# Kernel optimization log

Measured on AMD Instinct MI355X. Metric: run time of the kernel, lower is better.

Reference implementation:

```python
import jax, jax.numpy as jnp
import numpy as np

EPS = 1e-12  # torch F.normalize eps
K = 32       # num_clusters (hardcoded in module)

def l2norm(v, axis):
    n = jnp.sqrt(jnp.sum(v * v, axis=axis, keepdims=True))
    return v / jnp.maximum(n, EPS)

def setup_inputs() -> dict:
    key = jax.random.key(0)
    k1, k2, k3, k4 = jax.random.split(key, 4)
    B, M, D = 64, 128, 2048
    x = jax.random.normal(k1, (B, M, D), dtype=jnp.float32)
    # ragged lengths in [1, M]
    lengths = jax.random.randint(k2, (B,), 0, M, dtype=jnp.int32) + 1
    init_sc = 1.0 / np.sqrt(D)
    W = init_sc * jax.random.normal(k3, (K, D), dtype=jnp.float32)  # fc1.weight
    C = init_sc * jax.random.normal(k4, (K, D), dtype=jnp.float32)  # centroids
    return {"x": x, "lengths": lengths, "W": W, "C": C}

def reference(x, lengths, W, C):
    # x: [B,M,D] padded frames, lengths: [B] valid frame counts
    B, M, D = x.shape
    mask = (jnp.arange(M)[None, :] < lengths[:, None]).astype(x.dtype)  # [B,M]
    cnt = lengths.astype(x.dtype)[:, None]                              # [B,1]
    # avg pooling over valid (raw, un-normalized) frames
    avgpool = jnp.sum(x * mask[:, :, None], axis=1) / cnt               # [B,D]
    # per-frame L2 normalize
    xn = l2norm(x, axis=-1)                                             # [B,M,D]
    # soft assignment: linear (no bias) + softmax over clusters
    logits = jnp.einsum('bmd,kd->bmk', xn, W)
    a = jax.nn.softmax(logits, axis=-1) * mask[:, :, None]              # [B,M,K]
    # VLAD residual aggregation, GEMM form:
    # sum_m a[b,m,k]*(xn[b,m,:] - C[k,:]) = (a^T xn) - C * sum_m a
    ax = jnp.einsum('bmk,bmd->bkd', a, xn)                              # [B,K,D]
    asum = jnp.sum(a, axis=1)                                           # [B,K]
    vlad = ax - asum[:, :, None] * C[None, :, :]                        # [B,K,D]
    # intra-normalize per cluster, flatten, global L2 normalize
    vlad = l2norm(vlad, axis=2)
    vlad = vlad.reshape(B, K * D)
    vlad = l2norm(vlad, axis=1)
    return jnp.concatenate([avgpool, vlad], axis=1)                     # [B, D + K*D]
```

## Files before the change

### kernel.cpp

```cpp
#include <hip/hip_runtime.h>
#include <math.h>

#define BB 64
#define MM 128
#define DDIM 2048
#define KK 32
#define NFR (BB*MM)
#define OUTROW (DDIM + KK*DDIM)

typedef __attribute__((ext_vector_type(8))) short bf16x8;
typedef __attribute__((ext_vector_type(4))) float f32x4;

__device__ __forceinline__ short f2bf(float f) {
  unsigned u = __builtin_bit_cast(unsigned, f);
  u += 0x7fffu + ((u >> 16) & 1u);
  return (short)(u >> 16);
}
__device__ __forceinline__ unsigned pack2(float lo, float hi) {
  return (unsigned)(unsigned short)f2bf(lo) | ((unsigned)(unsigned short)f2bf(hi) << 16);
}

__global__ __launch_bounds__(256) void k_prep(const float* __restrict__ W,
                                              short* __restrict__ Wb) {
  int i = (blockIdx.x * 256 + threadIdx.x) * 8;
  float4 a = *(const float4*)(W + i);
  float4 b = *(const float4*)(W + i + 4);
  bf16x8 o = {f2bf(a.x), f2bf(a.y), f2bf(a.z), f2bf(a.w),
              f2bf(b.x), f2bf(b.y), f2bf(b.z), f2bf(b.w)};
  *(bf16x8*)(Wb + i) = o;
}

__global__ __launch_bounds__(256) void k_logits(const float* __restrict__ x,
    const int* __restrict__ lengths, const short* __restrict__ Wb,
    short* __restrict__ aT, float* __restrict__ asum_p) {
  const int t = threadIdx.x, wv = t >> 6, lane = t & 63;
  const int l15 = lane & 15, quad = lane >> 4;
  const int fg = blockIdx.x;
  const int g0 = fg * 16;
  const int b  = fg >> 3;
  const int m0 = (fg & 7) * 16;
  const int len = lengths[b];

  const float* xrow = x + (size_t)(g0 + l15) * DDIM + wv * 512 + quad * 8;
  const short* w0   = Wb + l15 * DDIM + wv * 512 + quad * 8;
  const short* w1   = w0 + 16 * DDIM;

  f32x4 c0 = {0.f, 0.f, 0.f, 0.f}, c1 = {0.f, 0.f, 0.f, 0.f};
  float ssq = 0.f;
  #pragma unroll
  for (int s = 0; s < 16; ++s) {
    float4 xa = *(const float4*)(xrow + s * 32);
    float4 xc = *(const float4*)(xrow + s * 32 + 4);
    ssq = fmaf(xa.x, xa.x, ssq); ssq = fmaf(xa.y, xa.y, ssq);
    ssq = fmaf(xa.z, xa.z, ssq); ssq = fmaf(xa.w, xa.w, ssq);
    ssq = fmaf(xc.x, xc.x, ssq); ssq = fmaf(xc.y, xc.y, ssq);
    ssq = fmaf(xc.z, xc.z, ssq); ssq = fmaf(xc.w, xc.w, ssq);
    bf16x8 A = {f2bf(xa.x), f2bf(xa.y), f2bf(xa.z), f2bf(xa.w),
                f2bf(xc.x), f2bf(xc.y), f2bf(xc.z), f2bf(xc.w)};
    bf16x8 B0 = *(const bf16x8*)(w0 + s * 32);
    bf16x8 B1 = *(const bf16x8*)(w1 + s * 32);
    c0 = __builtin_amdgcn_mfma_f32_16x16x32_bf16(A, B0, c0, 0, 0, 0);
    c1 = __builtin_amdgcn_mfma_f32_16x16x32_bf16(A, B1, c1, 0, 0, 0);
  }

  ssq += __shfl_xor(ssq, 16, 64);
  ssq += __shfl_xor(ssq, 32, 64);
  __shared__ float sq[4][16];
  __shared__ float lg[4][16][33];
  if (quad == 0) sq[wv][l15] = ssq;
  #pragma unroll
  for (int r = 0; r < 4; ++r) {
    lg[wv][quad * 4 + r][l15]      = c0[r];
    lg[wv][quad * 4 + r][16 + l15] = c1[r];
  }
  __syncthreads();

  const int fr = t >> 4, kk = (t & 15) * 2;
  float s0 = 0.f, s1 = 0.f;
  #pragma unroll
  for (int w = 0; w < 4; ++w) { s0 += lg[w][fr][kk]; s1 += lg[w][fr][kk + 1]; }
  float ss  = sq[0][fr] + sq[1][fr] + sq[2][fr] + sq[3][fr];
  float inv = 1.f / fmaxf(sqrtf(ss), 1e-12f);
  s0 *= inv; s1 *= inv;
  float mx = fmaxf(s0, s1);
  mx = fmaxf(mx, __shfl_xor(mx, 1, 64));
  mx = fmaxf(mx, __shfl_xor(mx, 2, 64));
  mx = fmaxf(mx, __shfl_xor(mx, 4, 64));
  mx = fmaxf(mx, __shfl_xor(mx, 8, 64));
  float e0 = __expf(s0 - mx), e1 = __expf(s1 - mx);
  float se = e0 + e1;
  se += __shfl_xor(se, 1, 64);
  se += __shfl_xor(se, 2, 64);
  se += __shfl_xor(se, 4, 64);
  se += __shfl_xor(se, 8, 64);
  const bool valid = (m0 + fr) < len;
  float rr = valid ? (1.f / se) : 0.f;
  float a0 = e0 * rr, a1 = e1 * rr;

  __syncthreads();
  lg[0][fr][kk] = a0; lg[0][fr][kk + 1] = a1;
  __syncthreads();
  if (t < KK) {
    float s = 0.f;
    #pragma unroll
    for (int f = 0; f < 16; ++f) s += lg[0][f][t];
    asum_p[(size_t)fg * KK + t] = s;
  }
  short* ap = aT + (size_t)b * KK * MM + m0 + fr;
  ap[(size_t)kk * MM]       = f2bf(a0 * inv);
  ap[(size_t)(kk + 1) * MM] = f2bf(a1 * inv);
}

__global__ __launch_bounds__(256) void k_vlad(const float* __restrict__ x,
    const int* __restrict__ lengths, const float* __restrict__ Cc,
    const short* __restrict__ aT, const float* __restrict__ asum_p,
    float* __restrict__ out, float* __restrict__ ssq_part) {
  const int t = threadIdx.x, wv = t >> 6, lane = t & 63;
  const int l15 = lane & 15, quad = lane >> 4;
  const int dc = blockIdx.x, b = blockIdx.y;
  const int dw0 = dc * 256 + wv * 64;
  const int len = lengths[b];

  __shared__ short xbt[4][64][40];
  __shared__ float asl[KK];
  __shared__ float ssw[4][33];

  if (t < KK) {
    float s = 0.f;
    #pragma unroll
    for (int p = 0; p < 8; ++p) s += asum_p[(size_t)(b * 8 + p) * KK + t];
    asl[t] = s;
  }

  const float* xb  = x  + (size_t)b * MM * DDIM;
  const short* at0 = aT + (size_t)b * KK * MM + l15 * MM + quad * 8;

  f32x4 acc[2][4];
  #pragma unroll
  for (int kt = 0; kt < 2; ++kt)
    #pragma unroll
    for (int nt = 0; nt < 4; ++nt) acc[kt][nt] = (f32x4){0.f, 0.f, 0.f, 0.f};
  float avg[4] = {0.f, 0.f, 0.f, 0.f};

  const int q4   = l15 * 4;
  const int mrow = (lane >> 4) * 2;

  for (int ms = 0; ms < 4; ++ms) {
    const int m0 = ms * 32;
    #pragma unroll
    for (int p = 0; p < 4; ++p) {
      int ml = p * 8 + mrow;
      int m  = m0 + ml;
      const float* xr = xb + (size_t)m * DDIM + dw0 + q4;
      float4 v0 = *(const float4*)xr;
      float4 v1 = *(const float4*)(xr + DDIM);
      float f0 = (m < len) ? 1.f : 0.f;
      float f1 = (m + 1 < len) ? 1.f : 0.f;
      avg[0] = fmaf(v0.x, f0, fmaf(v1.x, f1, avg[0]));
      avg[1] = fmaf(v0.y, f0, fmaf(v1.y, f1, avg[1]));
      avg[2] = fmaf(v0.z, f0, fmaf(v1.z, f1, avg[2]));
      avg[3] = fmaf(v0.w, f0, fmaf(v1.w, f1, avg[3]));
      *(unsigned*)&xbt[wv][q4 + 0][ml] = pack2(v0.x, v1.x);
      *(unsigned*)&xbt[wv][q4 + 1][ml] = pack2(v0.y, v1.y);
      *(unsigned*)&xbt[wv][q4 + 2][ml] = pack2(v0.z, v1.z);
      *(unsigned*)&xbt[wv][q4 + 3][ml] = pack2(v0.w, v1.w);
    }
    bf16x8 A0 = *(const bf16x8*)(at0 + m0);
    bf16x8 A1 = *(const bf16x8*)(at0 + 16 * MM + m0);
    #pragma unroll
    for (int nt = 0; nt < 4; ++nt) {
      bf16x8 B = *(const bf16x8*)&xbt[wv][nt * 16 + l15][quad * 8];
      acc[0][nt] = __builtin_amdgcn_mfma_f32_16x16x32_bf16(A0, B, acc[0][nt], 0, 0, 0);
      acc[1][nt] = __builtin_amdgcn_mfma_f32_16x16x32_bf16(A1, B, acc[1][nt], 0, 0, 0);
    }
  }

  #pragma unroll
  for (int c = 0; c < 4; ++c) {
    avg[c] += __shfl_xor(avg[c], 16, 64);
    avg[c] += __shfl_xor(avg[c], 32, 64);
  }
  if (quad == 0) {
    float rl = 1.f / (float)len;
    *(float4*)(out + (size_t)b * OUTROW + dw0 + q4) =
        make_float4(avg[0] * rl, avg[1] * rl, avg[2] * rl, avg[3] * rl);
  }

  __syncthreads();
  float* orow = out + (size_t)b * OUTROW + DDIM;
  #pragma unroll
  for (int kt = 0; kt < 2; ++kt) {
    #pragma unroll
    for (int r = 0; r < 4; ++r) {
      const int k = kt * 16 + quad * 4 + r;
      const float as = asl[k];
      float sqv = 0.f;
      #pragma unroll
      for (int nt = 0; nt < 4; ++nt) {
        const int d = dw0 + nt * 16 + l15;
        float v = acc[kt][nt][r] - as * Cc[(size_t)k * DDIM + d];
        orow[(size_t)k * DDIM + d] = v;
        sqv = fmaf(v, v, sqv);
      }
      sqv += __shfl_xor(sqv, 1, 64);
      sqv += __shfl_xor(sqv, 2, 64);
      sqv += __shfl_xor(sqv, 4, 64);
      sqv += __shfl_xor(sqv, 8, 64);
      if (l15 == 0) ssw[wv][k] = sqv;
    }
  }
  __syncthreads();
  if (t < KK)
    ssq_part[((size_t)dc * BB + b) * KK + t] =
        ssw[0][t] + ssw[1][t] + ssw[2][t] + ssw[3][t];
}

__global__ __launch_bounds__(256) void k_norm(const float* __restrict__ ssq_part,
    float* __restrict__ out) {
  const int t = threadIdx.x;
  const int k = blockIdx.x;
  const int b = blockIdx.y;
  __shared__ float ssk[32];
  if (t < 32) {
    float sk = 0.f;
    #pragma unroll
    for (int dc = 0; dc < 8; ++dc)
      sk += ssq_part[((size_t)dc * BB + b) * KK + t];
    ssk[t] = sk;
  }
  __syncthreads();
  float gss = 0.f, iv_own = 0.f;
  #pragma unroll
  for (int kk = 0; kk < 32; ++kk) {
    float nk = sqrtf(ssk[kk]);
    float iv = 1.f / fmaxf(nk, 1e-12f);
    float nn = nk * iv;
    gss += nn * nn;
    if (kk == k) iv_own = iv;
  }
  float sc = iv_own / fmaxf(sqrtf(gss), 1e-12f);
  float* row = out + (size_t)b * OUTROW + DDIM + (size_t)k * DDIM;
  #pragma unroll
  for (int h = 0; h < 2; ++h) {
    float4* p = (float4*)(row + h * 1024 + t * 4);
    float4 v = *p;
    v.x *= sc; v.y *= sc; v.z *= sc; v.w *= sc;
    *p = v;
  }
}

extern "C" void kernel_launch(void* const* d_in, const int* in_sizes, int n_in,
                              void* d_out, int out_size, void* d_ws, size_t ws_size,
                              hipStream_t stream) {
  const float* x       = (const float*)d_in[0];
  const int*   lengths = (const int*)d_in[1];
  const float* W       = (const float*)d_in[2];
  const float* C       = (const float*)d_in[3];
  float* out = (float*)d_out;

  short* Wb     = (short*)d_ws;
  short* aT     = Wb + (size_t)KK * DDIM;
  float* asum_p = (float*)(aT + (size_t)BB * KK * MM);
  float* ssqp   = asum_p + (size_t)512 * KK;

  k_prep  <<<dim3(32),     256, 0, stream>>>(W, Wb);
  k_logits<<<dim3(512),    256, 0, stream>>>(x, lengths, Wb, aT, asum_p);
  k_vlad  <<<dim3(8, BB),  256, 0, stream>>>(x, lengths, C, aT, asum_p, out, ssqp);
  k_norm  <<<dim3(KK, BB), 256, 0, stream>>>(ssqp, out);
}
```

Before: 146.1 us.

## Fuse W conversion into logits, split VLAD over cluster halves, skip padded frames

Drops the separate W-to-bf16 prep kernel and converts W inline in the logits kernel, which now runs 512 threads per block with each wave covering a narrower D slice. Loads of x for padded frames past each sequence length are skipped in both the logits and VLAD kernels. The VLAD kernel gains a third grid dimension that splits the 32 clusters into two halves, doubling block count but reading x twice. It also adds an XOR swizzle on the shared-memory transpose to reduce bank conflicts and preloads the assignment fragments.

Measured after the change: 176.9 us. +21.1%, slower.

```diff
diff --git a/kernel.cpp b/kernel.cpp
--- a/kernel.cpp
+++ b/kernel.cpp
@@ -16,22 +16,16 @@
   u += 0x7fffu + ((u >> 16) & 1u);
   return (short)(u >> 16);
 }
+__device__ __forceinline__ bf16x8 cvt8(float4 a, float4 b) {
+  return (bf16x8){f2bf(a.x), f2bf(a.y), f2bf(a.z), f2bf(a.w),
+                  f2bf(b.x), f2bf(b.y), f2bf(b.z), f2bf(b.w)};
+}
 __device__ __forceinline__ unsigned pack2(float lo, float hi) {
   return (unsigned)(unsigned short)f2bf(lo) | ((unsigned)(unsigned short)f2bf(hi) << 16);
 }
 
-__global__ __launch_bounds__(256) void k_prep(const float* __restrict__ W,
-                                              short* __restrict__ Wb) {
-  int i = (blockIdx.x * 256 + threadIdx.x) * 8;
-  float4 a = *(const float4*)(W + i);
-  float4 b = *(const float4*)(W + i + 4);
-  bf16x8 o = {f2bf(a.x), f2bf(a.y), f2bf(a.z), f2bf(a.w),
-              f2bf(b.x), f2bf(b.y), f2bf(b.z), f2bf(b.w)};
-  *(bf16x8*)(Wb + i) = o;
-}
-
-__global__ __launch_bounds__(256) void k_logits(const float* __restrict__ x,
-    const int* __restrict__ lengths, const short* __restrict__ Wb,
+__global__ __launch_bounds__(512, 4) void k_logits(const float* __restrict__ x,
+    const int* __restrict__ lengths, const float* __restrict__ W,
     short* __restrict__ aT, float* __restrict__ asum_p) {
   const int t = threadIdx.x, wv = t >> 6, lane = t & 63;
   const int l15 = lane & 15, quad = lane >> 4;
@@ -40,33 +34,41 @@
   const int b  = fg >> 3;
   const int m0 = (fg & 7) * 16;
   const int len = lengths[b];
-
-  const float* xrow = x + (size_t)(g0 + l15) * DDIM + wv * 512 + quad * 8;
-  const short* w0   = Wb + l15 * DDIM + wv * 512 + quad * 8;
-  const short* w1   = w0 + 16 * DDIM;
+  const bool av = (m0 + l15) < len;
+
+  const float* xrow = x + (size_t)(g0 + l15) * DDIM + wv * 256 + quad * 8;
+  const float* w0   = W + (size_t)l15 * DDIM + wv * 256 + quad * 8;
+  const float* w1   = w0 + 16 * DDIM;
 
   f32x4 c0 = {0.f, 0.f, 0.f, 0.f}, c1 = {0.f, 0.f, 0.f, 0.f};
   float ssq = 0.f;
   #pragma unroll
-  for (int s = 0; s < 16; ++s) {
-    float4 xa = *(const float4*)(xrow + s * 32);
-    float4 xc = *(const float4*)(xrow + s * 32 + 4);
+  for (int s = 0; s < 8; ++s) {
+    float4 xa = make_float4(0.f, 0.f, 0.f, 0.f);
+    float4 xc = make_float4(0.f, 0.f, 0.f, 0.f);
+    if (av) {
+      xa = *(const float4*)(xrow + s * 32);
+      xc = *(const float4*)(xrow + s * 32 + 4);
+    }
+    float4 wa0 = *(const float4*)(w0 + s * 32);
+    float4 wb0 = *(const float4*)(w0 + s * 32 + 4);
+    float4 wa1 = *(const float4*)(w1 + s * 32);
+    float4 wb1 = *(const float4*)(w1 + s * 32 + 4);
     ssq = fmaf(xa.x, xa.x, ssq); ssq = fmaf(xa.y, xa.y, ssq);
     ssq = fmaf(xa.z, xa.z, ssq); ssq = fmaf(xa.w, xa.w, ssq);
     ssq = fmaf(xc.x, xc.x, ssq); ssq = fmaf(xc.y, xc.y, ssq);
     ssq = fmaf(xc.z, xc.z, ssq); ssq = fmaf(xc.w, xc.w, ssq);
-    bf16x8 A = {f2bf(xa.x), f2bf(xa.y), f2bf(xa.z), f2bf(xa.w),
-                f2bf(xc.x), f2bf(xc.y), f2bf(xc.z), f2bf(xc.w)};
-    bf16x8 B0 = *(const bf16x8*)(w0 + s * 32);
-    bf16x8 B1 = *(const bf16x8*)(w1 + s * 32);
+    bf16x8 A  = cvt8(xa, xc);
+    bf16x8 B0 = cvt8(wa0, wb0);
+    bf16x8 B1 = cvt8(wa1, wb1);
     c0 = __builtin_amdgcn_mfma_f32_16x16x32_bf16(A, B0, c0, 0, 0, 0);
     c1 = __builtin_amdgcn_mfma_f32_16x16x32_bf16(A, B1, c1, 0, 0, 0);
   }
 
   ssq += __shfl_xor(ssq, 16, 64);
   ssq += __shfl_xor(ssq, 32, 64);
-  __shared__ float sq[4][16];
-  __shared__ float lg[4][16][33];
+  __shared__ float sq[8][16];
+  __shared__ float lg[8][16][33];
   if (quad == 0) sq[wv][l15] = ssq;
   #pragma unroll
   for (int r = 0; r < 4; ++r) {
@@ -75,30 +77,33 @@
   }
   __syncthreads();
 
-  const int fr = t >> 4, kk = (t & 15) * 2;
-  float s0 = 0.f, s1 = 0.f;
-  #pragma unroll
-  for (int w = 0; w < 4; ++w) { s0 += lg[w][fr][kk]; s1 += lg[w][fr][kk + 1]; }
-  float ss  = sq[0][fr] + sq[1][fr] + sq[2][fr] + sq[3][fr];
+  const int fr = t >> 5, kk = t & 31;
+  float s0 = 0.f;
+  #pragma unroll
+  for (int w = 0; w < 8; ++w) s0 += lg[w][fr][kk];
+  float ss = 0.f;
+  #pragma unroll
+  for (int w = 0; w < 8; ++w) ss += sq[w][fr];
   float inv = 1.f / fmaxf(sqrtf(ss), 1e-12f);
-  s0 *= inv; s1 *= inv;
-  float mx = fmaxf(s0, s1);
+  s0 *= inv;
+  float mx = s0;
   mx = fmaxf(mx, __shfl_xor(mx, 1, 64));
   mx = fmaxf(mx, __shfl_xor(mx, 2, 64));
   mx = fmaxf(mx, __shfl_xor(mx, 4, 64));
   mx = fmaxf(mx, __shfl_xor(mx, 8, 64));
-  float e0 = __expf(s0 - mx), e1 = __expf(s1 - mx);
-  float se = e0 + e1;
+  mx = fmaxf(mx, __shfl_xor(mx, 16, 64));
+  float e0 = __expf(s0 - mx);
+  float se = e0;
   se += __shfl_xor(se, 1, 64);
   se += __shfl_xor(se, 2, 64);
   se += __shfl_xor(se, 4, 64);
   se += __shfl_xor(se, 8, 64);
+  se += __shfl_xor(se, 16, 64);
   const bool valid = (m0 + fr) < len;
-  float rr = valid ? (1.f / se) : 0.f;
-  float a0 = e0 * rr, a1 = e1 * rr;
-
-  __syncthreads();
-  lg[0][fr][kk] = a0; lg[0][fr][kk + 1] = a1;
+  float a0 = valid ? (e0 / se) : 0.f;
+
+  __syncthreads();
+  lg[0][fr][kk] = a0;
   __syncthreads();
   if (t < KK) {
     float s = 0.f;
@@ -106,112 +111,115 @@
     for (int f = 0; f < 16; ++f) s += lg[0][f][t];
     asum_p[(size_t)fg * KK + t] = s;
   }
-  short* ap = aT + (size_t)b * KK * MM + m0 + fr;
-  ap[(size_t)kk * MM]       = f2bf(a0 * inv);
-  ap[(size_t)(kk + 1) * MM] = f2bf(a1 * inv);
-}
-
-__global__ __launch_bounds__(256) void k_vlad(const float* __restrict__ x,
+  aT[(size_t)b * KK * MM + (size_t)kk * MM + m0 + fr] = f2bf(a0 * inv);
+}
+
+__global__ __launch_bounds__(256, 4) void k_vlad(const float* __restrict__ x,
     const int* __restrict__ lengths, const float* __restrict__ Cc,
     const short* __restrict__ aT, const float* __restrict__ asum_p,
     float* __restrict__ out, float* __restrict__ ssq_part) {
   const int t = threadIdx.x, wv = t >> 6, lane = t & 63;
   const int l15 = lane & 15, quad = lane >> 4;
-  const int dc = blockIdx.x, b = blockIdx.y;
+  const int dc = blockIdx.x, b = blockIdx.y, ks = blockIdx.z;
+  const int k0 = ks * 16;
   const int dw0 = dc * 256 + wv * 64;
   const int len = lengths[b];
 
   __shared__ short xbt[4][64][40];
-  __shared__ float asl[KK];
-  __shared__ float ssw[4][33];
-
-  if (t < KK) {
+  __shared__ float asl[16];
+  __shared__ float ssw[4][16];
+
+  if (t < 16) {
     float s = 0.f;
     #pragma unroll
-    for (int p = 0; p < 8; ++p) s += asum_p[(size_t)(b * 8 + p) * KK + t];
+    for (int p = 0; p < 8; ++p) s += asum_p[(size_t)(b * 8 + p) * KK + k0 + t];
     asl[t] = s;
   }
 
   const float* xb  = x  + (size_t)b * MM * DDIM;
-  const short* at0 = aT + (size_t)b * KK * MM + l15 * MM + quad * 8;
-
-  f32x4 acc[2][4];
-  #pragma unroll
-  for (int kt = 0; kt < 2; ++kt)
-    #pragma unroll
-    for (int nt = 0; nt < 4; ++nt) acc[kt][nt] = (f32x4){0.f, 0.f, 0.f, 0.f};
+  const short* at0 = aT + (size_t)b * KK * MM + (size_t)(k0 + l15) * MM + quad * 8;
+
+  const int q4   = l15 * 4;
+  const int mrow = quad * 2;
+  const int keyw = l15 & 3;
+  const int keyr = (l15 >> 2) & 3;
+
+  bf16x8 A[4];
+  #pragma unroll
+  for (int ms = 0; ms < 4; ++ms) A[ms] = *(const bf16x8*)(at0 + ms * 32);
+
+  f32x4 acc[4];
+  #pragma unroll
+  for (int nt = 0; nt < 4; ++nt) acc[nt] = (f32x4){0.f, 0.f, 0.f, 0.f};
   float avg[4] = {0.f, 0.f, 0.f, 0.f};
 
-  const int q4   = l15 * 4;
-  const int mrow = (lane >> 4) * 2;
-
+  #pragma unroll
   for (int ms = 0; ms < 4; ++ms) {
-    const int m0 = ms * 32;
+    float4 v0[4], v1[4];
     #pragma unroll
     for (int p = 0; p < 4; ++p) {
-      int ml = p * 8 + mrow;
-      int m  = m0 + ml;
+      const int m = ms * 32 + p * 8 + mrow;
       const float* xr = xb + (size_t)m * DDIM + dw0 + q4;
-      float4 v0 = *(const float4*)xr;
-      float4 v1 = *(const float4*)(xr + DDIM);
-      float f0 = (m < len) ? 1.f : 0.f;
-      float f1 = (m + 1 < len) ? 1.f : 0.f;
-      avg[0] = fmaf(v0.x, f0, fmaf(v1.x, f1, avg[0]));
-      avg[1] = fmaf(v0.y, f0, fmaf(v1.y, f1, avg[1]));
-      avg[2] = fmaf(v0.z, f0, fmaf(v1.z, f1, avg[2]));
-      avg[3] = fmaf(v0.w, f0, fmaf(v1.w, f1, avg[3]));
-      *(unsigned*)&xbt[wv][q4 + 0][ml] = pack2(v0.x, v1.x);
-      *(unsigned*)&xbt[wv][q4 + 1][ml] = pack2(v0.y, v1.y);
-      *(unsigned*)&xbt[wv][q4 + 2][ml] = pack2(v0.z, v1.z);
-      *(unsigned*)&xbt[wv][q4 + 3][ml] = pack2(v0.w, v1.w);
-    }
-    bf16x8 A0 = *(const bf16x8*)(at0 + m0);
-    bf16x8 A1 = *(const bf16x8*)(at0 + 16 * MM + m0);
+      v0[p] = (m < len) ? *(const float4*)xr : make_float4(0.f, 0.f, 0.f, 0.f);
+      v1[p] = (m + 1 < len) ? *(const float4*)(xr + DDIM)
+                            : make_float4(0.f, 0.f, 0.f, 0.f);
+    }
+    #pragma unroll
+    for (int p = 0; p < 4; ++p) {
+      avg[0] += v0[p].x + v1[p].x;
+      avg[1] += v0[p].y + v1[p].y;
+      avg[2] += v0[p].z + v1[p].z;
+      avg[3] += v0[p].w + v1[p].w;
+      const int mls = (p ^ keyw) * 8 + mrow;
+      *(unsigned*)&xbt[wv][q4 + 0][mls] = pack2(v0[p].x, v1[p].x);
+      *(unsigned*)&xbt[wv][q4 + 1][mls] = pack2(v0[p].y, v1[p].y);
+      *(unsigned*)&xbt[wv][q4 + 2][mls] = pack2(v0[p].z, v1[p].z);
+      *(unsigned*)&xbt[wv][q4 + 3][mls] = pack2(v0[p].w, v1[p].w);
+    }
     #pragma unroll
     for (int nt = 0; nt < 4; ++nt) {
-      bf16x8 B = *(const bf16x8*)&xbt[wv][nt * 16 + l15][quad * 8];
-      acc[0][nt] = __builtin_amdgcn_mfma_f32_16x16x32_bf16(A0, B, acc[0][nt], 0, 0, 0);
-      acc[1][nt] = __builtin_amdgcn_mfma_f32_16x16x32_bf16(A1, B, acc[1][nt], 0, 0, 0);
-    }
-  }
-
-  #pragma unroll
-  for (int c = 0; c < 4; ++c) {
-    avg[c] += __shfl_xor(avg[c], 16, 64);
-    avg[c] += __shfl_xor(avg[c], 32, 64);
-  }
-  if (quad == 0) {
-    float rl = 1.f / (float)len;
-    *(float4*)(out + (size_t)b * OUTROW + dw0 + q4) =
-        make_float4(avg[0] * rl, avg[1] * rl, avg[2] * rl, avg[3] * rl);
+      bf16x8 B = *(const bf16x8*)&xbt[wv][nt * 16 + l15][(quad ^ keyr) * 8];
+      acc[nt] = __builtin_amdgcn_mfma_f32_16x16x32_bf16(A[ms], B, acc[nt], 0, 0, 0);
+    }
+  }
+
+  if (ks == 0) {
+    #pragma unroll
+    for (int c = 0; c < 4; ++c) {
+      avg[c] += __shfl_xor(avg[c], 16, 64);
+      avg[c] += __shfl_xor(avg[c], 32, 64);
+    }
+    if (quad == 0) {
+      float rl = 1.f / (float)len;
+      *(float4*)(out + (size_t)b * OUTROW + dw0 + q4) =
+          make_float4(avg[0] * rl, avg[1] * rl, avg[2] * rl, avg[3] * rl);
+    }
   }
 
   __syncthreads();
   float* orow = out + (size_t)b * OUTROW + DDIM;
   #pragma unroll
-  for (int kt = 0; kt < 2; ++kt) {
-    #pragma unroll
-    for (int r = 0; r < 4; ++r) {
-      const int k = kt * 16 + quad * 4 + r;
-      const float as = asl[k];
-      float sqv = 0.f;
-      #pragma unroll
-      for (int nt = 0; nt < 4; ++nt) {
-        const int d = dw0 + nt * 16 + l15;
-        float v = acc[kt][nt][r] - as * Cc[(size_t)k * DDIM + d];
-        orow[(size_t)k * DDIM + d] = v;
-        sqv = fmaf(v, v, sqv);
-      }
-      sqv += __shfl_xor(sqv, 1, 64);
-      sqv += __shfl_xor(sqv, 2, 64);
-      sqv += __shfl_xor(sqv, 4, 64);
-      sqv += __shfl_xor(sqv, 8, 64);
-      if (l15 == 0) ssw[wv][k] = sqv;
-    }
-  }
-  __syncthreads();
-  if (t < KK)
-    ssq_part[((size_t)dc * BB + b) * KK + t] =
+  for (int r = 0; r < 4; ++r) {
+    const int kl = quad * 4 + r;
+    const int k  = k0 + kl;
+    const float as = asl[kl];
+    float sqv = 0.f;
+    #pragma unroll
+    for (int nt = 0; nt < 4; ++nt) {
+      const int d = dw0 + nt * 16 + l15;
+      float v = acc[nt][r] - as * Cc[(size_t)k * DDIM + d];
+      orow[(size_t)k * DDIM + d] = v;
+      sqv = fmaf(v, v, sqv);
+    }
+    sqv += __shfl_xor(sqv, 1, 64);
+    sqv += __shfl_xor(sqv, 2, 64);
+    sqv += __shfl_xor(sqv, 4, 64);
+    sqv += __shfl_xor(sqv, 8, 64);
+    if (l15 == 0) ssw[wv][kl] = sqv;
+  }
+  __syncthreads();
+  if (t < 16)
+    ssq_part[((size_t)dc * BB + b) * KK + k0 + t] =
         ssw[0][t] + ssw[1][t] + ssw[2][t] + ssw[3][t];
 }
 
@@ -258,13 +266,11 @@
   const float* C       = (const float*)d_in[3];
   float* out = (float*)d_out;
 
-  short* Wb     = (short*)d_ws;
-  short* aT     = Wb + (size_t)KK * DDIM;
+  short* aT     = (short*)d_ws;
   float* asum_p = (float*)(aT + (size_t)BB * KK * MM);
   float* ssqp   = asum_p + (size_t)512 * KK;
 
-  k_prep  <<<dim3(32),     256, 0, stream>>>(W, Wb);
-  k_logits<<<dim3(512),    256, 0, stream>>>(x, lengths, Wb, aT, asum_p);
-  k_vlad  <<<dim3(8, BB),  256, 0, stream>>>(x, lengths, C, aT, asum_p, out, ssqp);
-  k_norm  <<<dim3(KK, BB), 256, 0, stream>>>(ssqp, out);
-}
+  k_logits<<<dim3(512),       512, 0, stream>>>(x, lengths, W, aT, asum_p);
+  k_vlad  <<<dim3(8, BB, 2),  256, 0, stream>>>(x, lengths, C, aT, asum_p, out, ssqp);
+  k_norm  <<<dim3(KK, BB),    256, 0, stream>>>(ssqp, out);
+}
```
